# Kernel optimization log

Hardware: AMD Instinct MI355X
Metric: run time of the kernel (lower is better)

## Reference

```python
import jax, jax.numpy as jnp
import numpy as np


def setup_inputs() -> dict:
    key = jax.random.key(0)
    k1, k2, k3, k4 = jax.random.split(key, 4)
    B, S, D = 8, 2048, 512
    scale = 1.0 / np.sqrt(D)
    return {
        "x": jax.random.normal(k1, (B, S, D), dtype=jnp.float32),
        "WQ": jax.random.normal(k2, (D, D), dtype=jnp.float32) * scale,
        "WK": jax.random.normal(k3, (D, D), dtype=jnp.float32) * scale,
        "WV": jax.random.normal(k4, (D, D), dtype=jnp.float32) * scale,
    }


def reference(x, WQ, WK, WV):
    # x: [B, S, D]; single-head scaled dot-product self-attention
    Q = jnp.einsum("bsd,de->bse", x, WQ)
    K = jnp.einsum("bsd,de->bse", x, WK)
    V = jnp.einsum("bsd,de->bse", x, WV)
    d_k = jnp.asarray(K.shape[-1], dtype=x.dtype)
    scores = jnp.einsum("bqd,bkd->bqk", Q, K) / jnp.sqrt(d_k)  # [B,S,S]
    weights = jax.nn.softmax(scores, axis=-1)
    return jnp.einsum("bqk,bkd->bqd", weights, V)
```

## Files before the change

kernel.cpp:

```cpp
#include <hip/hip_runtime.h>
#include <cstdint>
#include <cstddef>

#define B_ 8
#define S_ 2048
#define D_ 512

typedef float f32x4 __attribute__((ext_vector_type(4)));
typedef __bf16 bf16x8 __attribute__((ext_vector_type(8)));

__device__ __forceinline__ unsigned short f2bf(float f) {
    unsigned u = __builtin_bit_cast(unsigned, f);
    u += 0x7FFFu + ((u >> 16) & 1u);
    return (unsigned short)(u >> 16);
}

__device__ __forceinline__ void gll16(const void* g, void* l) {
    __builtin_amdgcn_global_load_lds(
        (const __attribute__((address_space(1))) unsigned int*)g,
        (__attribute__((address_space(3))) unsigned int*)l, 16, 0, 0);
}

#define VMCNT(n) asm volatile("s_waitcnt vmcnt(%0)" :: "i"(n) : "memory")
#define PHASE_FENCE() do { asm volatile("" ::: "memory"); \
                           __builtin_amdgcn_sched_barrier(0); } while (0)

template<int AMT, int BNT>
__global__ __launch_bounds__(512, 2) void gemm8(
    const unsigned short* __restrict__ A,
    const unsigned short* __restrict__ B,
    void* __restrict__ Cv,
    unsigned short* __restrict__ Cv2,
    float* __restrict__ rs_part,
    int K, int lda, int ldb, int ldc,
    long long sA, long long sB, long long sC,
    float scale, int mode, int ntn, int nbatch)
{
    constexpr int BM     = 64 * AMT;
    constexpr int BN     = 128 * BNT;
    constexpr int ABYTES = BM * 128;
    constexpr int BBYTES = BN * 128;
    constexpr int AH     = ABYTES / 2;
    constexpr int BH     = BBYTES / 2;
    constexpr int AGL    = AMT / 2;
    constexpr int BGL    = BNT;
    constexpr int BUFB   = ABYTES + BBYTES;
    __shared__ __align__(16) char lds[2 * BUFB];

    const int lin = blockIdx.x;
    const int bz  = lin % nbatch;
    const int tq  = lin / nbatch;
    const int tn  = tq % ntn;
    const int tm  = tq / ntn;
    A += (long long)bz * sA;
    B += (long long)bz * sB;
    const int m0   = tm * BM;
    const int n0   = tn * BN;
    const int tid  = threadIdx.x;
    const int lane = tid & 63;
    const int w    = tid >> 6;
    const int g2   = w >> 2;
    const int nb   = w & 3;

    const int lrow = lane >> 3;
    const int swz  = ((lane & 7) ^ lrow) << 3;
    const unsigned short* gA[2][AGL];
    const unsigned short* gB[2][BGL];
    #pragma unroll
    for (int h = 0; h < 2; ++h) {
        #pragma unroll
        for (int i = 0; i < AGL; ++i)
            gA[h][i] = A + (size_t)(m0 + h * (BM / 2) + (w * AGL + i) * 8 + lrow) * lda + swz;
        #pragma unroll
        for (int i = 0; i < BGL; ++i)
            gB[h][i] = B + (size_t)(n0 + h * (BN / 2) + (w * BGL + i) * 8 + lrow) * ldb + swz;
    }
    auto stA = [&](int bs, int h, int kof) {
        #pragma unroll
        for (int i = 0; i < AGL; ++i)
            gll16(gA[h][i] + kof, lds + bs * BUFB + h * AH + (w * AGL + i) * 1024);
    };
    auto stB = [&](int bs, int h, int kof) {
        #pragma unroll
        for (int i = 0; i < BGL; ++i)
            gll16(gB[h][i] + kof, lds + bs * BUFB + ABYTES + h * BH + (w * BGL + i) * 1024);
    };

    const int fr = lane & 15;
    const int gq = lane >> 4;
    const int c0 = (gq ^ (fr & 7)) << 4;
    int aoff[AMT], boff[BNT];
    #pragma unroll
    for (int ml = 0; ml < AMT; ++ml)
        aoff[ml] = (g2 * (16 * AMT) + ml * 16 + fr) * 128 + c0;
    #pragma unroll
    for (int nl = 0; nl < BNT; ++nl)
        boff[nl] = (nb * (16 * BNT) + nl * 16 + fr) * 128 + c0;

    bf16x8 af[2 * AMT], bLO[2 * BNT], bHI[2 * BNT];
    f32x4 acc[2 * AMT][2 * BNT] = {};

    auto ldA = [&](const char* Ab, int mh) {
        #pragma unroll
        for (int ml = 0; ml < AMT; ++ml)
            #pragma unroll
            for (int kk = 0; kk < 2; ++kk)
                af[ml * 2 + kk] = *(const bf16x8*)(Ab + mh * AH + (aoff[ml] ^ (kk << 6)));
    };
    auto ldB = [&](const char* Bb, int nh, bf16x8* bf) {
        #pragma unroll
        for (int nl = 0; nl < BNT; ++nl)
            #pragma unroll
            for (int kk = 0; kk < 2; ++kk)
                bf[nl * 2 + kk] = *(const bf16x8*)(Bb + nh * BH + (boff[nl] ^ (kk << 6)));
    };
    auto mma = [&](int mh, int nh, const bf16x8* bf) {
        __builtin_amdgcn_s_setprio(1);
        #pragma unroll
        for (int ml = 0; ml < AMT; ++ml)
            #pragma unroll
            for (int nl = 0; nl < BNT; ++nl)
                #pragma unroll
                for (int kk = 0; kk < 2; ++kk)
                    acc[mh * AMT + ml][nh * BNT + nl] =
                        __builtin_amdgcn_mfma_f32_16x16x32_bf16(
                            af[ml * 2 + kk], bf[nl * 2 + kk],
                            acc[mh * AMT + ml][nh * BNT + nl], 0, 0, 0);
        __builtin_amdgcn_s_setprio(0);
    };

    stA(0, 0, 0);  stB(0, 0, 0);
    stA(0, 1, 0);  stB(0, 1, 0);
    stA(1, 0, 64); stB(1, 0, 64);

    const int NT = K >> 6;
    for (int tt = 0; tt < NT; ++tt) {
        const int bs = tt & 1;
        const char* Ab = lds + bs * BUFB;
        const char* Bb = Ab + ABYTES;
        const bool last = (tt == NT - 1);

        if (!last) stA(bs ^ 1, 1, (tt + 1) << 6);
        if (last) { VMCNT(AGL + BGL); } else { VMCNT(6); }
        __builtin_amdgcn_s_barrier();
        PHASE_FENCE();
        ldA(Ab, 0); ldB(Bb, 0, bLO);
        mma(0, 0, bLO);

        if (!last) stB(bs ^ 1, 1, (tt + 1) << 6);
        if (last) { VMCNT(0); } else { VMCNT(6); }
        __builtin_amdgcn_s_barrier();
        PHASE_FENCE();
        ldB(Bb, 1, bHI);
        mma(0, 1, bHI);

        if (tt + 2 < NT) stA(bs, 0, (tt + 2) << 6);
        VMCNT(6);
        __builtin_amdgcn_s_barrier();
        PHASE_FENCE();
        ldA(Ab, 1);
        mma(1, 0, bLO);

        if (tt + 2 < NT) stB(bs, 0, (tt + 2) << 6);
        VMCNT(6);
        __builtin_amdgcn_s_barrier();
        PHASE_FENCE();
        mma(1, 1, bHI);
    }

    const int rb4 = gq << 2;
#define AB_(mt) ((((mt) / AMT) * (BM / 2)) + g2 * (16 * AMT) + ((mt) % AMT) * 16)
#define BB_(nt) ((((nt) / BNT) * (BN / 2)) + nb * (16 * BNT) + ((nt) % BNT) * 16)

    if (mode == 1) {
        #pragma unroll
        for (int mt = 0; mt < 2 * AMT; ++mt)
            #pragma unroll
            for (int nt = 0; nt < 2 * BNT; ++nt)
                #pragma unroll
                for (int r = 0; r < 4; ++r)
                    acc[mt][nt][r] = __expf(acc[mt][nt][r] * scale);

        unsigned short* C = (unsigned short*)Cv + (long long)bz * sC;
        #pragma unroll
        for (int mt = 0; mt < 2 * AMT; ++mt)
            #pragma unroll
            for (int nt = 0; nt < 2 * BNT; ++nt) {
                const int gc = n0 + BB_(nt) + fr;
                #pragma unroll
                for (int r = 0; r < 4; ++r)
                    C[(size_t)(m0 + AB_(mt) + rb4 + r) * ldc + gc] = f2bf(acc[mt][nt][r]);
            }

        float* rp = rs_part + (((long long)bz * S_) << 5) + tn * 4 + nb;
        #pragma unroll
        for (int mt = 0; mt < 2 * AMT; ++mt)
            #pragma unroll
            for (int r = 0; r < 4; ++r) {
                float s = 0.f;
                #pragma unroll
                for (int nt = 0; nt < 2 * BNT; ++nt) s += acc[mt][nt][r];
                s += __shfl_xor(s, 8);
                s += __shfl_xor(s, 4);
                s += __shfl_xor(s, 2);
                s += __shfl_xor(s, 1);
                if (fr == 0)
                    rp[(long long)(m0 + AB_(mt) + rb4 + r) << 5] = s;
            }
    } else if (mode == 3) {
        if (tn >= 4) {
            #pragma unroll
            for (int mt = 0; mt < 2 * AMT; ++mt) {
                const int s0q = m0 + AB_(mt) + rb4;
                const int b   = s0q >> 11;
                const int se  = s0q & (S_ - 1);
                #pragma unroll
                for (int nt = 0; nt < 2 * BNT; ++nt) {
                    const int d = (n0 - 2 * D_) + BB_(nt) + fr;
                    ushort4 u;
                    u.x = f2bf(acc[mt][nt][0]);
                    u.y = f2bf(acc[mt][nt][1]);
                    u.z = f2bf(acc[mt][nt][2]);
                    u.w = f2bf(acc[mt][nt][3]);
                    *(ushort4*)&Cv2[((size_t)b * D_ + d) * S_ + se] = u;
                }
            }
        } else {
            unsigned short* C = (unsigned short*)Cv;
            #pragma unroll
            for (int mt = 0; mt < 2 * AMT; ++mt)
                #pragma unroll
                for (int nt = 0; nt < 2 * BNT; ++nt) {
                    const int gc = n0 + BB_(nt) + fr;
                    #pragma unroll
                    for (int r = 0; r < 4; ++r)
                        C[(size_t)(m0 + AB_(mt) + rb4 + r) * ldc + gc] = f2bf(acc[mt][nt][r]);
                }
        }
    } else {
        float* C = (float*)Cv + (long long)bz * sC;
        #pragma unroll
        for (int nt = 0; nt < 2 * BNT; ++nt) {
            const int q = n0 + BB_(nt) + fr;
            const float* rp = rs_part + (((long long)bz * S_ + q) << 5);
            float ssum = 0.f;
            #pragma unroll
            for (int pq = 0; pq < 8; ++pq) {
                const float4 p4 = *(const float4*)(rp + 4 * pq);
                ssum += (p4.x + p4.y) + (p4.z + p4.w);
            }
            const float inv = __builtin_amdgcn_rcpf(ssum);
            #pragma unroll
            for (int mt = 0; mt < 2 * AMT; ++mt) {
                const int d0 = m0 + AB_(mt) + rb4;
                float4 o;
                o.x = acc[mt][nt][0] * inv;
                o.y = acc[mt][nt][1] * inv;
                o.z = acc[mt][nt][2] * inv;
                o.w = acc[mt][nt][3] * inv;
                *(float4*)&C[(size_t)q * ldc + d0] = o;
            }
        }
    }
#undef AB_
#undef BB_
}

__global__ __launch_bounds__(256) void convert_x4(const float* __restrict__ x,
                                                  unsigned short* __restrict__ xb) {
    const size_t i = ((size_t)blockIdx.x * 256 + threadIdx.x) * 4;
    const float4 f = *(const float4*)(x + i);
    ushort4 u;
    u.x = f2bf(f.x); u.y = f2bf(f.y); u.z = f2bf(f.z); u.w = f2bf(f.w);
    *(ushort4*)(xb + i) = u;
}

__global__ __launch_bounds__(256) void convert_w(const float* __restrict__ WQ,
                                                 const float* __restrict__ WK,
                                                 const float* __restrict__ WV,
                                                 unsigned short* __restrict__ WT) {
    const int o = blockIdx.x * 256 + threadIdx.x;
    const float* W = blockIdx.y == 0 ? WQ : (blockIdx.y == 1 ? WK : WV);
    const int e = o >> 9, d = o & (D_ - 1);
    WT[(size_t)blockIdx.y * D_ * D_ + o] = f2bf(W[d * D_ + e]);
}

extern "C" void kernel_launch(void* const* d_in, const int* in_sizes, int n_in,
                              void* d_out, int out_size, void* d_ws, size_t ws_size,
                              hipStream_t stream)
{
    const float* x  = (const float*)d_in[0];
    const float* WQ = (const float*)d_in[1];
    const float* WK = (const float*)d_in[2];
    const float* WV = (const float*)d_in[3];

    unsigned short* ws  = (unsigned short*)d_ws;
    const size_t NX = (size_t)B_ * S_ * D_;
    unsigned short* xb  = ws;
    unsigned short* wtb = xb + NX;
    unsigned short* qk  = wtb + 3 * D_ * D_;
    unsigned short* vtb = qk + NX * 2;
    unsigned short* sb  = vtb + NX;
    float* rsp = (float*)(sb + (size_t)B_ * S_ * S_);

    convert_x4<<<dim3((unsigned)(NX / 4 / 256)), 256, 0, stream>>>(x, xb);
    convert_w<<<dim3(D_ * D_ / 256, 3), 256, 0, stream>>>(WQ, WK, WV, wtb);

    gemm8<4, 2><<<dim3(384), 512, 0, stream>>>(
        xb, wtb, qk, vtb, nullptr, D_, D_, D_, 2 * D_,
        0, 0, 0, 1.0f, 3,  6,  1);

    gemm8<4, 2><<<dim3(512), 512, 0, stream>>>(
        qk , qk + D_ , sb, nullptr, rsp, D_, 2 * D_, 2 * D_, S_,
        (long long)S_ * 2 * D_, (long long)S_ * 2 * D_, (long long)S_ * S_,
        0.04419417382415922f, 1,  8,  8);

    gemm8<2, 2><<<dim3(256), 512, 0, stream>>>(
        vtb, sb, d_out, nullptr, rsp, S_, S_, S_, D_,
        (long long)D_ * S_, (long long)S_ * S_, (long long)S_ * D_,
        1.0f, 0,  8,  8);
}
```

Baseline: 228.2 us.

## Restructure GEMM K-loop pipeline to prefetch next tile after LDS reads

Reworks the software pipeline of the bf16 GEMM main loop. The prologue now loads only the first K tile and waits on it. Each phase issues its LDS fragment reads first, then the global-to-LDS prefetch of the next tile into the other buffer. Extra barriers are added around each MFMA block, with matching vmcnt waits. The goal is a simpler double-buffered schedule that overlaps the next tile's loads with MFMA work. The cost is prefetching only one tile ahead instead of two and roughly twice as many workgroup barriers per iteration, which may expose more memory latency.

```diff
diff --git a/kernel.cpp b/kernel.cpp
--- a/kernel.cpp
+++ b/kernel.cpp
@@ -22,8 +22,8 @@
 }
 
 #define VMCNT(n) asm volatile("s_waitcnt vmcnt(%0)" :: "i"(n) : "memory")
-#define PHASE_FENCE() do { asm volatile("" ::: "memory"); \
-                           __builtin_amdgcn_sched_barrier(0); } while (0)
+#define SBAR()   __builtin_amdgcn_s_barrier()
+#define SCHED0() __builtin_amdgcn_sched_barrier(0)
 
 template<int AMT, int BNT>
 __global__ __launch_bounds__(512, 2) void gemm8(
@@ -129,43 +129,54 @@
         __builtin_amdgcn_s_setprio(0);
     };
 
-    stA(0, 0, 0);  stB(0, 0, 0);
-    stA(0, 1, 0);  stB(0, 1, 0);
-    stA(1, 0, 64); stB(1, 0, 64);
+    stA(0, 0, 0); stB(0, 0, 0); stB(0, 1, 0); stA(0, 1, 0);
+    VMCNT(AGL + BGL);
+    SBAR();
+    SCHED0();
 
     const int NT = K >> 6;
     for (int tt = 0; tt < NT; ++tt) {
         const int bs = tt & 1;
         const char* Ab = lds + bs * BUFB;
         const char* Bb = Ab + ABYTES;
-        const bool last = (tt == NT - 1);
-
-        if (!last) stA(bs ^ 1, 1, (tt + 1) << 6);
-        if (last) { VMCNT(AGL + BGL); } else { VMCNT(6); }
-        __builtin_amdgcn_s_barrier();
-        PHASE_FENCE();
+        const int  nk  = (tt + 1) << 6;
+        const bool pf  = (tt + 1 < NT);
+
         ldA(Ab, 0); ldB(Bb, 0, bLO);
+        if (pf) stA(bs ^ 1, 0, nk);
+        SCHED0();
+        if (pf) { VMCNT(2 * AGL); } else { VMCNT(AGL); }
+        SBAR();
+        SCHED0();
         mma(0, 0, bLO);
-
-        if (!last) stB(bs ^ 1, 1, (tt + 1) << 6);
-        if (last) { VMCNT(0); } else { VMCNT(6); }
-        __builtin_amdgcn_s_barrier();
-        PHASE_FENCE();
+        SBAR();
+        SCHED0();
+
         ldB(Bb, 1, bHI);
+        if (pf) stB(bs ^ 1, 0, nk);
+        SCHED0();
+        if (pf) { VMCNT(AGL + BGL); } else { VMCNT(0); }
+        SBAR();
+        SCHED0();
         mma(0, 1, bHI);
-
-        if (tt + 2 < NT) stA(bs, 0, (tt + 2) << 6);
-        VMCNT(6);
-        __builtin_amdgcn_s_barrier();
-        PHASE_FENCE();
+        SBAR();
+        SCHED0();
+
         ldA(Ab, 1);
+        if (pf) stB(bs ^ 1, 1, nk);
+        SCHED0();
+        SBAR();
+        SCHED0();
         mma(1, 0, bLO);
-
-        if (tt + 2 < NT) stB(bs, 0, (tt + 2) << 6);
-        VMCNT(6);
-        __builtin_amdgcn_s_barrier();
-        PHASE_FENCE();
+        SBAR();
+        SCHED0();
+
+        if (pf) { stA(bs ^ 1, 1, nk); SCHED0(); VMCNT(AGL + BGL); }
+        SBAR();
+        SCHED0();
         mma(1, 1, bHI);
+        SBAR();
+        SCHED0();
     }
 
     const int rb4 = gq << 2;
```

Result: slower. 232.9 us (+2.1%).

## Fuse QK^T, softmax and PV into one flash-style attention kernel

Applied to the files above, without the earlier changes.

Replaces the separate score GEMM (which wrote bf16 exp-scores plus partial row sums to global memory) and the PV GEMM with a single fused kernel. For each 64-query tile it streams K and V chunks through double-buffered LDS, exponentiates scores in registers, stages P in LDS and accumulates PV, then normalises by row sums at the end. This removes the large S×S score matrix round trip through HBM and one kernel launch. It has no running max, so it relies on the small score range of these inputs, the same as before. Only 256 blocks run with large LDS use, which may limit occupancy. The projection GEMM tile also shrinks to 2x2 with 768 blocks.

```diff
diff --git a/kernel.cpp b/kernel.cpp
--- a/kernel.cpp
+++ b/kernel.cpp
@@ -22,8 +22,8 @@
 }
 
 #define VMCNT(n) asm volatile("s_waitcnt vmcnt(%0)" :: "i"(n) : "memory")
-#define PHASE_FENCE() do { asm volatile("" ::: "memory"); \
-                           __builtin_amdgcn_sched_barrier(0); } while (0)
+#define SBAR()   __builtin_amdgcn_s_barrier()
+#define SCHED0() __builtin_amdgcn_sched_barrier(0)
 
 template<int AMT, int BNT>
 __global__ __launch_bounds__(512, 2) void gemm8(
@@ -143,28 +143,28 @@
         if (!last) stA(bs ^ 1, 1, (tt + 1) << 6);
         if (last) { VMCNT(AGL + BGL); } else { VMCNT(6); }
         __builtin_amdgcn_s_barrier();
-        PHASE_FENCE();
+        SCHED0();
         ldA(Ab, 0); ldB(Bb, 0, bLO);
         mma(0, 0, bLO);
 
         if (!last) stB(bs ^ 1, 1, (tt + 1) << 6);
         if (last) { VMCNT(0); } else { VMCNT(6); }
         __builtin_amdgcn_s_barrier();
-        PHASE_FENCE();
+        SCHED0();
         ldB(Bb, 1, bHI);
         mma(0, 1, bHI);
 
         if (tt + 2 < NT) stA(bs, 0, (tt + 2) << 6);
         VMCNT(6);
         __builtin_amdgcn_s_barrier();
-        PHASE_FENCE();
+        SCHED0();
         ldA(Ab, 1);
         mma(1, 0, bLO);
 
         if (tt + 2 < NT) stB(bs, 0, (tt + 2) << 6);
         VMCNT(6);
         __builtin_amdgcn_s_barrier();
-        PHASE_FENCE();
+        SCHED0();
         mma(1, 1, bHI);
     }
 
@@ -172,42 +172,7 @@
 #define AB_(mt) ((((mt) / AMT) * (BM / 2)) + g2 * (16 * AMT) + ((mt) % AMT) * 16)
 #define BB_(nt) ((((nt) / BNT) * (BN / 2)) + nb * (16 * BNT) + ((nt) % BNT) * 16)
 
-    if (mode == 1) {
-        #pragma unroll
-        for (int mt = 0; mt < 2 * AMT; ++mt)
-            #pragma unroll
-            for (int nt = 0; nt < 2 * BNT; ++nt)
-                #pragma unroll
-                for (int r = 0; r < 4; ++r)
-                    acc[mt][nt][r] = __expf(acc[mt][nt][r] * scale);
-
-        unsigned short* C = (unsigned short*)Cv + (long long)bz * sC;
-        #pragma unroll
-        for (int mt = 0; mt < 2 * AMT; ++mt)
-            #pragma unroll
-            for (int nt = 0; nt < 2 * BNT; ++nt) {
-                const int gc = n0 + BB_(nt) + fr;
-                #pragma unroll
-                for (int r = 0; r < 4; ++r)
-                    C[(size_t)(m0 + AB_(mt) + rb4 + r) * ldc + gc] = f2bf(acc[mt][nt][r]);
-            }
-
-        float* rp = rs_part + (((long long)bz * S_) << 5) + tn * 4 + nb;
-        #pragma unroll
-        for (int mt = 0; mt < 2 * AMT; ++mt)
-            #pragma unroll
-            for (int r = 0; r < 4; ++r) {
-                float s = 0.f;
-                #pragma unroll
-                for (int nt = 0; nt < 2 * BNT; ++nt) s += acc[mt][nt][r];
-                s += __shfl_xor(s, 8);
-                s += __shfl_xor(s, 4);
-                s += __shfl_xor(s, 2);
-                s += __shfl_xor(s, 1);
-                if (fr == 0)
-                    rp[(long long)(m0 + AB_(mt) + rb4 + r) << 5] = s;
-            }
-    } else if (mode == 3) {
+    if (mode == 3) {
         if (tn >= 4) {
             #pragma unroll
             for (int mt = 0; mt < 2 * AMT; ++mt) {
@@ -237,33 +202,157 @@
                         C[(size_t)(m0 + AB_(mt) + rb4 + r) * ldc + gc] = f2bf(acc[mt][nt][r]);
                 }
         }
-    } else {
-        float* C = (float*)Cv + (long long)bz * sC;
-        #pragma unroll
-        for (int nt = 0; nt < 2 * BNT; ++nt) {
-            const int q = n0 + BB_(nt) + fr;
-            const float* rp = rs_part + (((long long)bz * S_ + q) << 5);
-            float ssum = 0.f;
-            #pragma unroll
-            for (int pq = 0; pq < 8; ++pq) {
-                const float4 p4 = *(const float4*)(rp + 4 * pq);
-                ssum += (p4.x + p4.y) + (p4.z + p4.w);
-            }
-            const float inv = __builtin_amdgcn_rcpf(ssum);
-            #pragma unroll
-            for (int mt = 0; mt < 2 * AMT; ++mt) {
-                const int d0 = m0 + AB_(mt) + rb4;
-                float4 o;
-                o.x = acc[mt][nt][0] * inv;
-                o.y = acc[mt][nt][1] * inv;
-                o.z = acc[mt][nt][2] * inv;
-                o.w = acc[mt][nt][3] * inv;
-                *(float4*)&C[(size_t)q * ldc + d0] = o;
-            }
-        }
     }
 #undef AB_
 #undef BB_
+}
+
+__global__ __launch_bounds__(512, 2) void fused_attn(
+    const unsigned short* __restrict__ qk,
+    const unsigned short* __restrict__ vtb,
+    float* __restrict__ out,
+    float scale)
+{
+    __shared__ __align__(16) char lds[115712];
+    char* const PB = lds + 98304;
+    float* const RS = (float*)(lds + 114688);
+
+    const int lin = blockIdx.x;
+    const int bz  = lin & 7;
+    const int q0  = (lin >> 3) * 64;
+    const int tid = threadIdx.x;
+    const int lane = tid & 63;
+    const int w   = tid >> 6;
+    const int fr  = lane & 15;
+    const int gq  = lane >> 4;
+    const int g2  = w >> 2;
+    const int nb  = w & 3;
+
+    int row4[4], sc4[4];
+    #pragma unroll
+    for (int i = 0; i < 4; ++i) {
+        const int off = tid * 16 + i * 8192;
+        row4[i] = off >> 8;
+        sc4[i]  = ((((off >> 4) & 15) ^ (row4[i] & 7)) << 3);
+    }
+    const size_t qrowb = (size_t)bz * S_;
+
+    auto stK = [&](int b, int kv0, int j) {
+        #pragma unroll
+        for (int i = 0; i < 4; ++i)
+            gll16(qk + (qrowb + kv0 + row4[i]) * 1024 + 512 + j * 128 + sc4[i],
+                  lds + b * 49152 + tid * 16 + i * 8192);
+    };
+    auto stQ = [&](int b, int j) {
+        #pragma unroll
+        for (int i = 0; i < 2; ++i)
+            gll16(qk + (qrowb + q0 + row4[i]) * 1024 + j * 128 + sc4[i],
+                  lds + b * 49152 + 32768 + tid * 16 + i * 8192);
+    };
+    auto stV = [&](int b, int kv0, int c) {
+        #pragma unroll
+        for (int i = 0; i < 4; ++i)
+            gll16(vtb + ((size_t)bz * D_ + c * 128 + row4[i]) * S_ + kv0 + sc4[i],
+                  lds + b * 49152 + tid * 16 + i * 8192);
+    };
+
+    f32x4 acc_pv[4][4] = {};
+    float rsl = 0.f;
+    const int k7 = fr & 7;
+
+    stK(0, 0, 0); stQ(0, 0);
+    __syncthreads();
+    int cur = 0;
+
+    for (int kvi = 0; kvi < 16; ++kvi) {
+        const int kv0 = kvi * 128;
+
+        f32x4 acc_s[4] = {};
+        #pragma unroll
+        for (int j = 0; j < 4; ++j) {
+            if (j < 3) { stK(cur ^ 1, kv0, j + 1); stQ(cur ^ 1, j + 1); }
+            else       { stV(cur ^ 1, kv0, 0); }
+            const char* Kb = lds + cur * 49152;
+            const char* Qb = Kb + 32768;
+            #pragma unroll
+            for (int kk = 0; kk < 4; ++kk) {
+                const int ch = ((kk * 4 + gq) ^ k7) << 4;
+                const bf16x8 qf = *(const bf16x8*)(Qb + (nb * 16 + fr) * 256 + ch);
+                #pragma unroll
+                for (int mt = 0; mt < 4; ++mt) {
+                    const bf16x8 kf = *(const bf16x8*)(
+                        Kb + (g2 * 64 + mt * 16 + fr) * 256 + ch);
+                    acc_s[mt] = __builtin_amdgcn_mfma_f32_16x16x32_bf16(
+                        kf, qf, acc_s[mt], 0, 0, 0);
+                }
+            }
+            __syncthreads();
+            cur ^= 1;
+        }
+
+        #pragma unroll
+        for (int mt = 0; mt < 4; ++mt) {
+            float p0 = __expf(acc_s[mt][0] * scale);
+            float p1 = __expf(acc_s[mt][1] * scale);
+            float p2 = __expf(acc_s[mt][2] * scale);
+            float p3 = __expf(acc_s[mt][3] * scale);
+            rsl += (p0 + p1) + (p2 + p3);
+            ushort4 u;
+            u.x = f2bf(p0); u.y = f2bf(p1); u.z = f2bf(p2); u.w = f2bf(p3);
+            const int chunk = g2 * 8 + mt * 2 + (gq >> 1);
+            *(ushort4*)(PB + (nb * 16 + fr) * 256 +
+                        ((chunk ^ k7) << 4) + (gq & 1) * 8) = u;
+        }
+        __syncthreads();
+
+        bf16x8 pf[4][4];
+        #pragma unroll
+        for (int nt2 = 0; nt2 < 4; ++nt2)
+            #pragma unroll
+            for (int ks = 0; ks < 4; ++ks)
+                pf[nt2][ks] = *(const bf16x8*)(
+                    PB + (nt2 * 16 + fr) * 256 + (((ks * 4 + gq) ^ k7) << 4));
+
+        #pragma unroll
+        for (int c = 0; c < 4; ++c) {
+            if (c < 3)          stV(cur ^ 1, kv0, c + 1);
+            else if (kvi < 15) { stK(cur ^ 1, kv0 + 128, 0); stQ(cur ^ 1, 0); }
+            const char* Vb = lds + cur * 49152;
+            #pragma unroll
+            for (int ks = 0; ks < 4; ++ks) {
+                const bf16x8 vf = *(const bf16x8*)(
+                    Vb + (w * 16 + fr) * 256 + (((ks * 4 + gq) ^ k7) << 4));
+                #pragma unroll
+                for (int nt2 = 0; nt2 < 4; ++nt2)
+                    acc_pv[c][nt2] = __builtin_amdgcn_mfma_f32_16x16x32_bf16(
+                        vf, pf[nt2][ks], acc_pv[c][nt2], 0, 0, 0);
+            }
+            __syncthreads();
+            cur ^= 1;
+        }
+    }
+
+    rsl += __shfl_xor(rsl, 16);
+    rsl += __shfl_xor(rsl, 32);
+    if (lane < 16) RS[g2 * 64 + nb * 16 + lane] = rsl;
+    __syncthreads();
+
+    #pragma unroll
+    for (int nt2 = 0; nt2 < 4; ++nt2) {
+        const int q = nt2 * 16 + fr;
+        const float inv = __builtin_amdgcn_rcpf(RS[q] + RS[64 + q]);
+        float* op = out + ((qrowb + q0 + q) * D_);
+        #pragma unroll
+        for (int c = 0; c < 4; ++c) {
+            const int d0 = c * 128 + w * 16 + gq * 4;
+            float4 o;
+            o.x = acc_pv[c][nt2][0] * inv;
+            o.y = acc_pv[c][nt2][1] * inv;
+            o.z = acc_pv[c][nt2][2] * inv;
+            o.w = acc_pv[c][nt2][3] * inv;
+            *(float4*)(op + d0) = o;
+        }
+    }
 }
 
 __global__ __launch_bounds__(256) void convert_x4(const float* __restrict__ x,
@@ -300,23 +389,14 @@
     unsigned short* wtb = xb + NX;
     unsigned short* qk  = wtb + 3 * D_ * D_;
     unsigned short* vtb = qk + NX * 2;
-    unsigned short* sb  = vtb + NX;
-    float* rsp = (float*)(sb + (size_t)B_ * S_ * S_);
 
     convert_x4<<<dim3((unsigned)(NX / 4 / 256)), 256, 0, stream>>>(x, xb);
     convert_w<<<dim3(D_ * D_ / 256, 3), 256, 0, stream>>>(WQ, WK, WV, wtb);
 
-    gemm8<4, 2><<<dim3(384), 512, 0, stream>>>(
+    gemm8<2, 2><<<dim3(768), 512, 0, stream>>>(
         xb, wtb, qk, vtb, nullptr, D_, D_, D_, 2 * D_,
         0, 0, 0, 1.0f, 3,  6,  1);
 
-    gemm8<4, 2><<<dim3(512), 512, 0, stream>>>(
-        qk , qk + D_ , sb, nullptr, rsp, D_, 2 * D_, 2 * D_, S_,
-        (long long)S_ * 2 * D_, (long long)S_ * 2 * D_, (long long)S_ * S_,
-        0.04419417382415922f, 1,  8,  8);
-
-    gemm8<2, 2><<<dim3(256), 512, 0, stream>>>(
-        vtb, sb, d_out, nullptr, rsp, S_, S_, S_, D_,
-        (long long)D_ * S_, (long long)S_ * S_, (long long)S_ * D_,
-        1.0f, 0,  8,  8);
-}
+    fused_attn<<<dim3(256), 512, 0, stream>>>(
+        qk, vtb, (float*)d_out, 0.04419417382415922f);
+}
```

Result: slower. 244.7 us (+7.2%).
